# Optimization experiments

Measured on AMD Instinct MI355X. Metric: run time of the kernel, lower is better.

Reference implementation:

```python
import jax, jax.numpy as jnp
import numpy as np

B, S, D, H = 4, 2048, 512, 8
HD = D // H  # head_dim = 64


def setup_inputs() -> dict:
    key = jax.random.key(0)
    ks = jax.random.split(key, 16)
    sd = 1.0 / np.sqrt(D)
    def lin(ka, kb):
        W = jax.random.uniform(ka, (D, D), jnp.float32, -sd, sd)
        b = jax.random.uniform(kb, (D,), jnp.float32, -sd, sd)
        return W, b
    Wq, bq = lin(ks[0], ks[1])
    Wk, bk = lin(ks[2], ks[3])
    Wv, bv = lin(ks[4], ks[5])
    Wo, bo = lin(ks[6], ks[7])
    Ws, bs = lin(ks[8], ks[9])
    Wsh, bsh = lin(ks[10], ks[11])
    mod1_feat = jax.random.normal(ks[12], (B, S, D), jnp.float32)
    mod2_feat = jax.random.normal(ks[13], (B, S, D), jnp.float32)
    return {"mod1_feat": mod1_feat, "mod2_feat": mod2_feat,
            "Wq": Wq, "bq": bq, "Wk": Wk, "bk": bk, "Wv": Wv, "bv": bv,
            "Wo": Wo, "bo": bo, "Ws": Ws, "bs": bs, "Wsh": Wsh, "bsh": bsh}


def _heads(x):
    # [B, S, D] -> [B, H, S, HD]
    b, s, _ = x.shape
    return x.reshape(b, s, H, HD).transpose(0, 2, 1, 3)


def reference(mod1_feat, mod2_feat, Wq, bq, Wk, bk, Wv, bv, Wo, bo, Ws, bs, Wsh, bsh):
    Q = _heads(mod1_feat @ Wq + bq)
    K = _heads(mod2_feat @ Wk + bk)
    V = _heads(mod2_feat @ Wv + bv)
    scale = _heads(mod2_feat @ Ws + bs)
    shift = _heads(mod2_feat @ Wsh + bsh)
    K = K * scale + shift
    V = V * scale + shift
    scores = jnp.einsum('bhqd,bhkd->bhqk', Q, K) / jnp.sqrt(jnp.float32(HD))
    attn = jax.nn.softmax(scores, axis=-1)
    out = jnp.einsum('bhqk,bhkd->bhqd', attn, V)  # [B, H, S, HD]
    out = out.transpose(0, 2, 1, 3).reshape(mod1_feat.shape[0], -1, H * HD)
    return out @ Wo + bo
```

## Files before the change

### kernel.cpp

```cpp
#include <hip/hip_runtime.h>
#include <hip/hip_bf16.h>
#include <cstdint>
#include <cstddef>

typedef __bf16 bf16_t;
typedef __bf16 bf16x8 __attribute__((ext_vector_type(8)));
typedef __bf16 bf16x4 __attribute__((ext_vector_type(4)));
typedef float f32x4 __attribute__((ext_vector_type(4)));

#define DEVINL static __device__ __forceinline__

constexpr int B_ = 4, S_ = 2048, D_ = 512, H_ = 8, HD_ = 64;
constexpr int M_ = B_ * S_;
constexpr int NIN = 14;

DEVINL bf16x8 load8g(const bf16_t* p) { return *reinterpret_cast<const bf16x8*>(p); }

DEVINL int swcol(int col, int row) {
  return (col & ~63) | ((((col >> 3) ^ row) & 7) << 3) | (col & 7);
}

DEVINL int pK(int row) { return (row & 3) | (((row >> 3) & 1) << 2); }
DEVINL int swcolK(int col, int row) {
  return (col & ~63) | ((((col >> 3) ^ pK(row)) & 7) << 3) | (col & 7);
}

DEVINL void gl2lds(const bf16_t* g, bf16_t* l) {
  __builtin_amdgcn_global_load_lds(
      (const __attribute__((address_space(1))) void*)g,
      (__attribute__((address_space(3))) void*)l, 16, 0, 0);
}

DEVINL void stage16(bf16_t* dst, const void* src, size_t off, bool f32) {
  if (f32) {
    const float* p = (const float*)src + off;
    bf16x8 v0, v1;
#pragma unroll
    for (int j = 0; j < 8; ++j) { v0[j] = (bf16_t)p[j]; v1[j] = (bf16_t)p[8 + j]; }
    *reinterpret_cast<bf16x8*>(dst)     = v0;
    *reinterpret_cast<bf16x8*>(dst + 8) = v1;
  } else {
    const bf16_t* p = (const bf16_t*)src + off;
    *reinterpret_cast<bf16x8*>(dst)     = load8g(p);
    *reinterpret_cast<bf16x8*>(dst + 8) = load8g(p + 8);
  }
}

DEVINL float readf(const void* p, size_t i, bool f32) {
  return f32 ? ((const float*)p)[i] : (float)((const bf16_t*)p)[i];
}

struct DetectArgs { const uint16_t* p[NIN]; int n[NIN]; int* flags; };

__global__ __launch_bounds__(64) void detect_kernel(DetectArgs a) {
  const int z = blockIdx.x;
  const uint16_t* p = a.p[z];
  const int n = a.n[z];
  const int t = threadIdx.x;
  int cnt = 0;
  for (int i = t; i < n; i += 64) {
    const int e = (p[i] >> 7) & 0xFF;
    cnt += (e >= 200);
  }
#pragma unroll
  for (int off = 32; off > 0; off >>= 1) cnt += __shfl_down(cnt, off, 64);
  if (t == 0) a.flags[z] = (cnt > 16) ? 1 : 0;
}

struct CvtArgs { const void* src[2]; bf16_t* dst[2]; int idx[2]; const int* flags; };

__global__ __launch_bounds__(256) void cvt_kernel(CvtArgs a) {
  const int z = blockIdx.y;
  const bool f32 = a.flags[a.idx[z]] != 0;
  const size_t i = ((size_t)blockIdx.x * 256 + threadIdx.x) * 8;
  const int row = (int)(i >> 9);
  const int col = (int)(i & 511);
  bf16_t* dst = a.dst[z] + (size_t)row * 512 + swcol(col, row);
  if (f32) {
    const float* p = (const float*)a.src[z] + i;
    bf16x8 v;
#pragma unroll
    for (int j = 0; j < 8; ++j) v[j] = (bf16_t)p[j];
    *reinterpret_cast<bf16x8*>(dst) = v;
  } else {
    *reinterpret_cast<bf16x8*>(dst) = load8g((const bf16_t*)a.src[z] + i);
  }
}

struct TransArgs { const void* src[6]; int srcIdx[6]; bf16_t* dst[6]; const int* flags; };

__global__ __launch_bounds__(256) void transpose_kernel(TransArgs a) {
  __shared__ bf16_t tile[64][80];
  const int w = blockIdx.z;
  const void* src = a.src[w];
  const bool f32 = a.flags[a.srcIdx[w]] != 0;
  bf16_t* dst = a.dst[w];
  const int k0 = blockIdx.x * 64, n0 = blockIdx.y * 64;
  const int t = threadIdx.x;
  const int r = t >> 2, c0 = (t & 3) * 16;
  stage16(&tile[r][c0], src, (size_t)(k0 + r) * 512 + n0 + c0, f32);
  __syncthreads();
  const int orow = n0 + r;
  bf16_t* o = dst + (size_t)orow * 512;
#pragma unroll
  for (int half = 0; half < 2; ++half) {
    bf16x8 ov;
#pragma unroll
    for (int j = 0; j < 8; ++j) ov[j] = tile[c0 + half * 8 + j][r];
    *reinterpret_cast<bf16x8*>(o + swcol(k0 + c0 + half * 8, orow)) = ov;
  }
}

struct GemmBatch {
  const bf16_t* A[3];
  const bf16_t* Bt[3];
  const void* bias[3]; int bIdx[3];
  void* C[3];          int cIdx[3];
  const int* flags;
};

__global__ __launch_bounds__(512) void gemm_bt_kernel(GemmBatch args) {
  constexpr int K = 512, N = 512;
  __shared__ bf16_t As[3][128][64];
  __shared__ bf16_t Bs[3][64][64];
  const int z = blockIdx.z;
  const bf16_t* Ag  = args.A[z];
  const bf16_t* Btg = args.Bt[z];
  const int m0 = blockIdx.x * 128, n0 = blockIdx.y * 64;
  const int t = threadIdx.x, lane = t & 63, wave = t >> 6;
  const int l16 = lane & 15, quad = lane >> 4;
  const int wm = wave * 16;
  const int lr = lane >> 3, lc = (lane & 7) * 8;

  auto stage = [&](int slot, int k0) {
#pragma unroll
    for (int s = 0; s < 2; ++s) {
      const int r = wm + s * 8;
      gl2lds(Ag + (size_t)(m0 + r + lr) * K + k0 + lc, &As[slot][r][0]);
    }
    gl2lds(Btg + (size_t)(n0 + wave * 8 + lr) * K + k0 + lc, &Bs[slot][wave * 8][0]);
  };

  f32x4 acc[4] = {};

  stage(0, 0);
  stage(1, 64);

  constexpr int NT = K / 64;
  int cur = 0;
  for (int kt = 0; kt < NT - 1; ++kt) {
    asm volatile("s_waitcnt vmcnt(3)\n\ts_barrier" ::: "memory");
    __builtin_amdgcn_sched_barrier(0);
    if (kt + 2 < NT) {
      const int slot2 = cur == 0 ? 2 : cur - 1;
      stage(slot2, (kt + 2) * 64);
    }
#pragma unroll
    for (int ks = 0; ks < 2; ++ks) {
      const int sw = swcol(ks * 32 + quad * 8, l16);
      bf16x8 af = *reinterpret_cast<const bf16x8*>(&As[cur][wm + l16][sw]);
      bf16x8 bfr[4];
#pragma unroll
      for (int j = 0; j < 4; ++j)
        bfr[j] = *reinterpret_cast<const bf16x8*>(&Bs[cur][j * 16 + l16][sw]);
#pragma unroll
      for (int j = 0; j < 4; ++j)
        acc[j] = __builtin_amdgcn_mfma_f32_16x16x32_bf16(af, bfr[j], acc[j], 0, 0, 0);
    }
    cur = (cur == 2) ? 0 : cur + 1;
  }
  asm volatile("s_waitcnt vmcnt(0)\n\ts_barrier" ::: "memory");
  __builtin_amdgcn_sched_barrier(0);
#pragma unroll
  for (int ks = 0; ks < 2; ++ks) {
    const int sw = swcol(ks * 32 + quad * 8, l16);
    bf16x8 af = *reinterpret_cast<const bf16x8*>(&As[cur][wm + l16][sw]);
    bf16x8 bfr[4];
#pragma unroll
    for (int j = 0; j < 4; ++j)
      bfr[j] = *reinterpret_cast<const bf16x8*>(&Bs[cur][j * 16 + l16][sw]);
#pragma unroll
    for (int j = 0; j < 4; ++j)
      acc[j] = __builtin_amdgcn_mfma_f32_16x16x32_bf16(af, bfr[j], acc[j], 0, 0, 0);
  }

  const void* biag = args.bias[z];
  void* Cg         = args.C[z];
  const bool bf32 = args.bIdx[z] >= 0 && args.flags[args.bIdx[z]];
  const bool cf32 = args.cIdx[z] >= 0 && args.flags[args.cIdx[z]];
#pragma unroll
  for (int j = 0; j < 4; ++j) {
    const int col = n0 + j * 16 + l16;
    const float bv = readf(biag, col, bf32);
    const int rowb = m0 + wm + quad * 4;
#pragma unroll
    for (int r = 0; r < 4; ++r) {
      const size_t idx = (size_t)(rowb + r) * N + col;
      const float v = acc[j][r] + bv;
      if (cf32) ((float*)Cg)[idx] = v;
      else      ((bf16_t*)Cg)[idx] = (bf16_t)v;
    }
  }
}

struct GemmModArgs {
  const bf16_t* A;
  const bf16_t* Bt[2];
  const void* bias[2]; int bIdx[2];
  const bf16_t* Sc;
  const bf16_t* Sh;
  bf16_t* Kmod;
  bf16_t* VtT;
  const int* flags;
};

__global__ __launch_bounds__(512) void gemm_mod_kernel(GemmModArgs args) {
  constexpr int K = 512;
  __shared__ bf16_t As[3][128][64];
  __shared__ bf16_t Bs[3][64][64];
  const int z = blockIdx.z;
  const bf16_t* Ag  = args.A;
  const bf16_t* Btg = args.Bt[z];
  const int m0 = blockIdx.x * 128, n0 = blockIdx.y * 64;
  const int t = threadIdx.x, lane = t & 63, wave = t >> 6;
  const int l16 = lane & 15, quad = lane >> 4;
  const int wm = wave * 16;
  const int lr = lane >> 3, lc = (lane & 7) * 8;

  auto stage = [&](int slot, int k0) {
#pragma unroll
    for (int s = 0; s < 2; ++s) {
      const int r = wm + s * 8;
      gl2lds(Ag + (size_t)(m0 + r + lr) * K + k0 + lc, &As[slot][r][0]);
    }
    gl2lds(Btg + (size_t)(n0 + wave * 8 + lr) * K + k0 + lc, &Bs[slot][wave * 8][0]);
  };

  f32x4 acc[4] = {};

  stage(0, 0);
  stage(1, 64);

  constexpr int NT = K / 64;
  int cur = 0;
  for (int kt = 0; kt < NT - 1; ++kt) {
    asm volatile("s_waitcnt vmcnt(3)\n\ts_barrier" ::: "memory");
    __builtin_amdgcn_sched_barrier(0);
    if (kt + 2 < NT) {
      const int slot2 = cur == 0 ? 2 : cur - 1;
      stage(slot2, (kt + 2) * 64);
    }
#pragma unroll
    for (int ks = 0; ks < 2; ++ks) {
      const int sw = swcol(ks * 32 + quad * 8, l16);
      bf16x8 af = *reinterpret_cast<const bf16x8*>(&As[cur][wm + l16][sw]);
      bf16x8 bfr[4];
#pragma unroll
      for (int j = 0; j < 4; ++j)
        bfr[j] = *reinterpret_cast<const bf16x8*>(&Bs[cur][j * 16 + l16][sw]);
#pragma unroll
      for (int j = 0; j < 4; ++j)
        acc[j] = __builtin_amdgcn_mfma_f32_16x16x32_bf16(af, bfr[j], acc[j], 0, 0, 0);
    }
    cur = (cur == 2) ? 0 : cur + 1;
  }
  asm volatile("s_waitcnt vmcnt(0)\n\ts_barrier" ::: "memory");
  __builtin_amdgcn_sched_barrier(0);
#pragma unroll
  for (int ks = 0; ks < 2; ++ks) {
    const int sw = swcol(ks * 32 + quad * 8, l16);
    bf16x8 af = *reinterpret_cast<const bf16x8*>(&As[cur][wm + l16][sw]);
    bf16x8 bfr[4];
#pragma unroll
    for (int j = 0; j < 4; ++j)
      bfr[j] = *reinterpret_cast<const bf16x8*>(&Bs[cur][j * 16 + l16][sw]);
#pragma unroll
    for (int j = 0; j < 4; ++j)
      acc[j] = __builtin_amdgcn_mfma_f32_16x16x32_bf16(af, bfr[j], acc[j], 0, 0, 0);
  }

  const void* biag = args.bias[z];
  const bool bf32 = args.bIdx[z] >= 0 && args.flags[args.bIdx[z]];
#pragma unroll
  for (int j = 0; j < 4; ++j) {
    const int col = n0 + j * 16 + l16;
    const float bv = readf(biag, col, bf32);
    const int rowb = m0 + wm + quad * 4;
    if (z == 0) {
#pragma unroll
      for (int r = 0; r < 4; ++r) {
        const int row = rowb + r;
        const size_t idx = (size_t)row * 512 + col;
        const float sc = (float)args.Sc[idx], sh = (float)args.Sh[idx];
        args.Kmod[(size_t)row * 512 + swcolK(col, row)] = (bf16_t)fmaf(acc[j][r] + bv, sc, sh);
      }
    } else {
      bf16x4 pack;
#pragma unroll
      for (int r = 0; r < 4; ++r) {
        const size_t idx = (size_t)(rowb + r) * 512 + col;
        const float sc = (float)args.Sc[idx], sh = (float)args.Sh[idx];
        pack[r] = (bf16_t)fmaf(acc[j][r] + bv, sc, sh);
      }
      const int bb = rowb >> 11;
      const int ss = rowb & 2047;
      const int hh = col >> 6, dd = col & 63;
      *reinterpret_cast<bf16x4*>(
          args.VtT + (((size_t)(bb * H_ + hh)) * HD_ + dd) * S_ + swcol(ss, dd)) = pack;
    }
  }
}

__global__ __launch_bounds__(512) void attn_kernel(const bf16_t* Q, const bf16_t* Kb,
                                                   const bf16_t* Vt, bf16_t* O) {
  __shared__ bf16_t Ks[3][64][64];
  __shared__ bf16_t Vs[3][64][64];
  const int i = blockIdx.x;
  const int xcd = i & 7, g = i >> 3;
  const int slice = xcd * 4 + (g & 3);
  const int qt = g >> 2;
  const int b = slice >> 3, h = slice & 7;
  const int t = threadIdx.x, wave = t >> 6, lane = t & 63;
  const int l16 = lane & 15, quad = lane >> 4;
  const int q0 = qt * 128 + wave * 16;
  const int lr = lane >> 3, lc = (lane & 7) * 8;

  bf16x8 ones;
#pragma unroll
  for (int j = 0; j < 8; ++j) ones[j] = (bf16_t)1.0f;

  bf16x8 qf[2];
  {
    const size_t qrow = ((size_t)b * S_ + q0 + l16) * D_ + h * HD_;
    qf[0] = load8g(Q + qrow + quad * 8);
    qf[1] = load8g(Q + qrow + 32 + quad * 8);
  }

  f32x4 oacc[4] = {};
  f32x4 lacc = {};

  const size_t kbase = (size_t)b * S_ * D_ + h * HD_;
  const size_t vbase = ((size_t)(b * H_ + h)) * HD_ * S_;

  const int rbase = ((l16 >> 2) << 3) | (l16 & 3);
  int koff[2][4];
#pragma unroll
  for (int j = 0; j < 4; ++j) {
    const int rho = rbase + (j >> 1) * 32 + (j & 1) * 4;
#pragma unroll
    for (int dc = 0; dc < 2; ++dc)
      koff[dc][j] = rho * 64 + swcolK(dc * 32 + quad * 8, rho);
  }
  const int voff[2] = { swcol(quad * 8, l16), swcol(32 + quad * 8, l16) };

  auto stage = [&](int slot, int k0) {
    const int r = wave * 8;
    gl2lds(Kb + kbase + (size_t)(k0 + r + lr) * D_ + lc, &Ks[slot][r][0]);
    gl2lds(Vt + vbase + (size_t)(r + lr) * S_ + k0 + lc, &Vs[slot][r][0]);
  };

  constexpr float CE = 0.18033688011112042f;

  auto compute = [&](int cur) {
    f32x4 sacc[4] = {};
    const bf16_t* ksbase = &Ks[cur][0][0];
#pragma unroll
    for (int dc = 0; dc < 2; ++dc) {
      bf16x8 kf[4];
#pragma unroll
      for (int j = 0; j < 4; ++j)
        kf[j] = *reinterpret_cast<const bf16x8*>(ksbase + koff[dc][j]);
#pragma unroll
      for (int j = 0; j < 4; ++j)
        sacc[j] = __builtin_amdgcn_mfma_f32_16x16x32_bf16(kf[j], qf[dc], sacc[j], 0, 0, 0);
    }
#pragma unroll
    for (int kc = 0; kc < 2; ++kc) {
      bf16x8 vf[4];
#pragma unroll
      for (int dj = 0; dj < 4; ++dj)
        vf[dj] = *reinterpret_cast<const bf16x8*>(&Vs[cur][dj * 16 + l16][voff[kc]]);
      bf16x8 bp;
#pragma unroll
      for (int r = 0; r < 4; ++r) {
        bp[r]     = (bf16_t)__builtin_amdgcn_exp2f(fminf(sacc[kc * 2][r]     * CE, 57.5f));
        bp[4 + r] = (bf16_t)__builtin_amdgcn_exp2f(fminf(sacc[kc * 2 + 1][r] * CE, 57.5f));
      }
#pragma unroll
      for (int dj = 0; dj < 4; ++dj)
        oacc[dj] = __builtin_amdgcn_mfma_f32_16x16x32_bf16(vf[dj], bp, oacc[dj], 0, 0, 0);
      lacc = __builtin_amdgcn_mfma_f32_16x16x32_bf16(ones, bp, lacc, 0, 0, 0);
    }
  };

  asm volatile("s_waitcnt vmcnt(0)" ::: "memory");
  stage(0, 0);
  stage(1, 64);

  constexpr int NT = S_ / 64;
  int cur = 0;
  for (int kt = 0; kt < NT - 1; ++kt) {
    asm volatile("s_waitcnt vmcnt(2)\n\ts_barrier" ::: "memory");
    __builtin_amdgcn_sched_barrier(0);
    if (kt + 2 < NT) {
      const int slot2 = cur == 0 ? 2 : cur - 1;
      stage(slot2, (kt + 2) * 64);
    }
    compute(cur);
    cur = (cur == 2) ? 0 : cur + 1;
  }
  asm volatile("s_waitcnt vmcnt(0)\n\ts_barrier" ::: "memory");
  __builtin_amdgcn_sched_barrier(0);
  compute(cur);

  {
    const float linv = 1.0f / fmaxf(lacc[0], 1e-30f);
    const int q = q0 + l16;
    const size_t orow = ((size_t)b * S_ + q) * D_ + h * HD_;
#pragma unroll
    for (int dj = 0; dj < 4; ++dj) {
      bf16x4 pack;
#pragma unroll
      for (int r = 0; r < 4; ++r) pack[r] = (bf16_t)(oacc[dj][r] * linv);
      *reinterpret_cast<bf16x4*>(&O[orow + swcol(dj * 16 + quad * 4, q)]) = pack;
    }
  }
}

extern "C" void kernel_launch(void* const* d_in, const int* in_sizes, int n_in,
                              void* d_out, int out_size, void* d_ws, size_t ws_size,
                              hipStream_t stream) {
  (void)n_in; (void)out_size; (void)ws_size;

  char* ws = (char*)d_ws;
  auto alloc = [&](size_t bytes) -> char* {
    char* p = ws; ws += (bytes + 255) & ~(size_t)255; return p;
  };
  int* flags = (int*)alloc(64 * sizeof(int));
  const size_t wbytes = (size_t)512 * 512 * sizeof(bf16_t);
  const size_t fbytes = (size_t)M_ * D_ * sizeof(bf16_t);
  bf16_t* wt    = (bf16_t*)alloc(6 * wbytes);
  bf16_t* m1b   = (bf16_t*)alloc(fbytes);
  bf16_t* m2b   = (bf16_t*)alloc(fbytes);
  bf16_t* q_buf = (bf16_t*)alloc(fbytes);
  bf16_t* stmp  = (bf16_t*)alloc(fbytes);
  bf16_t* shtmp = (bf16_t*)alloc(fbytes);
  bf16_t* kmod  = (bf16_t*)alloc(fbytes);
  bf16_t* vtb    = m1b;
  bf16_t* attn_b = stmp;

  bf16_t* wtq  = wt + 0 * 512 * 512;
  bf16_t* wtk  = wt + 1 * 512 * 512;
  bf16_t* wtv  = wt + 2 * 512 * 512;
  bf16_t* wts  = wt + 3 * 512 * 512;
  bf16_t* wtsh = wt + 4 * 512 * 512;
  bf16_t* wto  = wt + 5 * 512 * 512;

  DetectArgs da;
  for (int i = 0; i < NIN; ++i) {
    da.p[i] = (const uint16_t*)d_in[i];
    da.n[i] = in_sizes[i] < 2048 ? in_sizes[i] : 2048;
  }
  da.flags = flags;
  hipLaunchKernelGGL(detect_kernel, dim3(NIN), dim3(64), 0, stream, da);

  CvtArgs ca;
  ca.src[0] = d_in[0]; ca.dst[0] = m1b; ca.idx[0] = 0;
  ca.src[1] = d_in[1]; ca.dst[1] = m2b; ca.idx[1] = 1;
  ca.flags = flags;
  hipLaunchKernelGGL(cvt_kernel, dim3(M_ * D_ / 2048, 2), dim3(256), 0, stream, ca);

  TransArgs ta;
  const int widx[6] = {2, 4, 6, 10, 12, 8};
  bf16_t* wdst[6] = {wtq, wtk, wtv, wts, wtsh, wto};
  for (int i = 0; i < 6; ++i) { ta.src[i] = d_in[widx[i]]; ta.srcIdx[i] = widx[i]; ta.dst[i] = wdst[i]; }
  ta.flags = flags;
  hipLaunchKernelGGL(transpose_kernel, dim3(8, 8, 6), dim3(256), 0, stream, ta);

  GemmBatch g1;
  g1.A[0] = m1b; g1.A[1] = m2b; g1.A[2] = m2b;
  g1.Bt[0] = wtq; g1.Bt[1] = wts; g1.Bt[2] = wtsh;
  g1.bias[0] = d_in[3];  g1.bIdx[0] = 3;
  g1.bias[1] = d_in[11]; g1.bIdx[1] = 11;
  g1.bias[2] = d_in[13]; g1.bIdx[2] = 13;
  g1.C[0] = q_buf; g1.cIdx[0] = -1;
  g1.C[1] = stmp;  g1.cIdx[1] = -1;
  g1.C[2] = shtmp; g1.cIdx[2] = -1;
  g1.flags = flags;
  hipLaunchKernelGGL(gemm_bt_kernel, dim3(M_ / 128, 8, 3), dim3(512), 0, stream, g1);

  GemmModArgs gm;
  gm.A = m2b;
  gm.Bt[0] = wtk; gm.Bt[1] = wtv;
  gm.bias[0] = d_in[5]; gm.bIdx[0] = 5;
  gm.bias[1] = d_in[7]; gm.bIdx[1] = 7;
  gm.Sc = stmp; gm.Sh = shtmp;
  gm.Kmod = kmod; gm.VtT = vtb;
  gm.flags = flags;
  hipLaunchKernelGGL(gemm_mod_kernel, dim3(M_ / 128, 8, 2), dim3(512), 0, stream, gm);

  hipLaunchKernelGGL(attn_kernel, dim3(512), dim3(512), 0, stream,
                     q_buf, kmod, vtb, attn_b);

  GemmBatch g2;
  for (int i = 0; i < 3; ++i) {
    g2.A[i] = attn_b;
    g2.Bt[i] = wto;
    g2.bias[i] = d_in[9]; g2.bIdx[i] = 9;
    g2.C[i] = d_out; g2.cIdx[i] = 0;
  }
  g2.flags = flags;
  hipLaunchKernelGGL(gemm_bt_kernel, dim3(M_ / 128, 8, 1), dim3(512), 0, stream, g2);
}
```

Measured before the change: 215.3 us.

## Fuse K, V, scale and shift projections into one GEMM with in-register modulation

```diff
diff --git a/kernel.cpp b/kernel.cpp
--- a/kernel.cpp
+++ b/kernel.cpp
@@ -203,40 +203,42 @@
   }
 }
 
-struct GemmModArgs {
+struct KsvArgs {
   const bf16_t* A;
-  const bf16_t* Bt[2];
-  const void* bias[2]; int bIdx[2];
-  const bf16_t* Sc;
-  const bf16_t* Sh;
+  const bf16_t* Bt[4];
+  const void* bias[4]; int bIdx[4];
   bf16_t* Kmod;
   bf16_t* VtT;
   const int* flags;
 };
 
-__global__ __launch_bounds__(512) void gemm_mod_kernel(GemmModArgs args) {
+__global__ __launch_bounds__(512) void ksv_kernel(KsvArgs args) {
   constexpr int K = 512;
   __shared__ bf16_t As[3][128][64];
-  __shared__ bf16_t Bs[3][64][64];
-  const int z = blockIdx.z;
-  const bf16_t* Ag  = args.A;
-  const bf16_t* Btg = args.Bt[z];
+  __shared__ bf16_t Bs[3][4][64][64];
   const int m0 = blockIdx.x * 128, n0 = blockIdx.y * 64;
   const int t = threadIdx.x, lane = t & 63, wave = t >> 6;
   const int l16 = lane & 15, quad = lane >> 4;
-  const int wm = wave * 16;
+  const int wm = (wave >> 2) * 64;
+  const int wn = (wave & 3) * 16;
   const int lr = lane >> 3, lc = (lane & 7) * 8;
 
   auto stage = [&](int slot, int k0) {
 #pragma unroll
     for (int s = 0; s < 2; ++s) {
-      const int r = wm + s * 8;
-      gl2lds(Ag + (size_t)(m0 + r + lr) * K + k0 + lc, &As[slot][r][0]);
-    }
-    gl2lds(Btg + (size_t)(n0 + wave * 8 + lr) * K + k0 + lc, &Bs[slot][wave * 8][0]);
+      const int r = wave * 16 + s * 8;
+      gl2lds(args.A + (size_t)(m0 + r + lr) * K + k0 + lc, &As[slot][r][0]);
+    }
+    const int mat = wave >> 1;
+    const int rb = (wave & 1) * 32;
+#pragma unroll
+    for (int s = 0; s < 4; ++s) {
+      const int r = rb + s * 8;
+      gl2lds(args.Bt[mat] + (size_t)(n0 + r + lr) * K + k0 + lc, &Bs[slot][mat][r][0]);
+    }
   };
 
-  f32x4 acc[4] = {};
+  f32x4 acc[4][4] = {};
 
   stage(0, 0);
   stage(1, 64);
@@ -244,7 +246,7 @@
   constexpr int NT = K / 64;
   int cur = 0;
   for (int kt = 0; kt < NT - 1; ++kt) {
-    asm volatile("s_waitcnt vmcnt(3)\n\ts_barrier" ::: "memory");
+    asm volatile("s_waitcnt vmcnt(6)\n\ts_barrier" ::: "memory");
     __builtin_amdgcn_sched_barrier(0);
     if (kt + 2 < NT) {
       const int slot2 = cur == 0 ? 2 : cur - 1;
@@ -253,14 +255,18 @@
 #pragma unroll
     for (int ks = 0; ks < 2; ++ks) {
       const int sw = swcol(ks * 32 + quad * 8, l16);
-      bf16x8 af = *reinterpret_cast<const bf16x8*>(&As[cur][wm + l16][sw]);
-      bf16x8 bfr[4];
-#pragma unroll
-      for (int j = 0; j < 4; ++j)
-        bfr[j] = *reinterpret_cast<const bf16x8*>(&Bs[cur][j * 16 + l16][sw]);
-#pragma unroll
-      for (int j = 0; j < 4; ++j)
-        acc[j] = __builtin_amdgcn_mfma_f32_16x16x32_bf16(af, bfr[j], acc[j], 0, 0, 0);
+      bf16x8 af[4], bfr[4];
+#pragma unroll
+      for (int mi = 0; mi < 4; ++mi)
+        af[mi] = *reinterpret_cast<const bf16x8*>(&As[cur][wm + mi * 16 + l16][sw]);
+#pragma unroll
+      for (int mat = 0; mat < 4; ++mat)
+        bfr[mat] = *reinterpret_cast<const bf16x8*>(&Bs[cur][mat][wn + l16][sw]);
+#pragma unroll
+      for (int mat = 0; mat < 4; ++mat)
+#pragma unroll
+        for (int mi = 0; mi < 4; ++mi)
+          acc[mat][mi] = __builtin_amdgcn_mfma_f32_16x16x32_bf16(af[mi], bfr[mat], acc[mat][mi], 0, 0, 0);
     }
     cur = (cur == 2) ? 0 : cur + 1;
   }
@@ -269,45 +275,44 @@
 #pragma unroll
   for (int ks = 0; ks < 2; ++ks) {
     const int sw = swcol(ks * 32 + quad * 8, l16);
-    bf16x8 af = *reinterpret_cast<const bf16x8*>(&As[cur][wm + l16][sw]);
-    bf16x8 bfr[4];
-#pragma unroll
-    for (int j = 0; j < 4; ++j)
-      bfr[j] = *reinterpret_cast<const bf16x8*>(&Bs[cur][j * 16 + l16][sw]);
-#pragma unroll
-    for (int j = 0; j < 4; ++j)
-      acc[j] = __builtin_amdgcn_mfma_f32_16x16x32_bf16(af, bfr[j], acc[j], 0, 0, 0);
-  }
-
-  const void* biag = args.bias[z];
-  const bool bf32 = args.bIdx[z] >= 0 && args.flags[args.bIdx[z]];
-#pragma unroll
-  for (int j = 0; j < 4; ++j) {
-    const int col = n0 + j * 16 + l16;
-    const float bv = readf(biag, col, bf32);
-    const int rowb = m0 + wm + quad * 4;
-    if (z == 0) {
-#pragma unroll
-      for (int r = 0; r < 4; ++r) {
-        const int row = rowb + r;
-        const size_t idx = (size_t)row * 512 + col;
-        const float sc = (float)args.Sc[idx], sh = (float)args.Sh[idx];
-        args.Kmod[(size_t)row * 512 + swcolK(col, row)] = (bf16_t)fmaf(acc[j][r] + bv, sc, sh);
-      }
-    } else {
-      bf16x4 pack;
-#pragma unroll
-      for (int r = 0; r < 4; ++r) {
-        const size_t idx = (size_t)(rowb + r) * 512 + col;
-        const float sc = (float)args.Sc[idx], sh = (float)args.Sh[idx];
-        pack[r] = (bf16_t)fmaf(acc[j][r] + bv, sc, sh);
-      }
-      const int bb = rowb >> 11;
-      const int ss = rowb & 2047;
-      const int hh = col >> 6, dd = col & 63;
-      *reinterpret_cast<bf16x4*>(
-          args.VtT + (((size_t)(bb * H_ + hh)) * HD_ + dd) * S_ + swcol(ss, dd)) = pack;
-    }
+    bf16x8 af[4], bfr[4];
+#pragma unroll
+    for (int mi = 0; mi < 4; ++mi)
+      af[mi] = *reinterpret_cast<const bf16x8*>(&As[cur][wm + mi * 16 + l16][sw]);
+#pragma unroll
+    for (int mat = 0; mat < 4; ++mat)
+      bfr[mat] = *reinterpret_cast<const bf16x8*>(&Bs[cur][mat][wn + l16][sw]);
+#pragma unroll
+    for (int mat = 0; mat < 4; ++mat)
+#pragma unroll
+      for (int mi = 0; mi < 4; ++mi)
+        acc[mat][mi] = __builtin_amdgcn_mfma_f32_16x16x32_bf16(af[mi], bfr[mat], acc[mat][mi], 0, 0, 0);
+  }
+
+  const int col = n0 + wn + l16;
+  const float bk  = readf(args.bias[0], col, args.bIdx[0] >= 0 && args.flags[args.bIdx[0]]);
+  const float bv  = readf(args.bias[1], col, args.bIdx[1] >= 0 && args.flags[args.bIdx[1]]);
+  const float bs  = readf(args.bias[2], col, args.bIdx[2] >= 0 && args.flags[args.bIdx[2]]);
+  const float bsh = readf(args.bias[3], col, args.bIdx[3] >= 0 && args.flags[args.bIdx[3]]);
+  const int hh = col >> 6, dd = col & 63;
+#pragma unroll
+  for (int mi = 0; mi < 4; ++mi) {
+    const int rowb = m0 + wm + mi * 16 + quad * 4;
+    bf16x4 vpack;
+#pragma unroll
+    for (int r = 0; r < 4; ++r) {
+      const int row = rowb + r;
+      const float s  = acc[2][mi][r] + bs;
+      const float sh = acc[3][mi][r] + bsh;
+      const float kk = fmaf(acc[0][mi][r] + bk, s, sh);
+      const float vv = fmaf(acc[1][mi][r] + bv, s, sh);
+      args.Kmod[(size_t)row * 512 + swcolK(col, row)] = (bf16_t)kk;
+      vpack[r] = (bf16_t)vv;
+    }
+    const int bb = rowb >> 11;
+    const int ss = rowb & 2047;
+    *reinterpret_cast<bf16x4*>(
+        args.VtT + (((size_t)(bb * H_ + hh)) * HD_ + dd) * S_ + swcol(ss, dd)) = vpack;
   }
 }
 
@@ -443,11 +448,10 @@
   bf16_t* m1b   = (bf16_t*)alloc(fbytes);
   bf16_t* m2b   = (bf16_t*)alloc(fbytes);
   bf16_t* q_buf = (bf16_t*)alloc(fbytes);
-  bf16_t* stmp  = (bf16_t*)alloc(fbytes);
-  bf16_t* shtmp = (bf16_t*)alloc(fbytes);
+  bf16_t* atmp  = (bf16_t*)alloc(fbytes);
   bf16_t* kmod  = (bf16_t*)alloc(fbytes);
   bf16_t* vtb    = m1b;
-  bf16_t* attn_b = stmp;
+  bf16_t* attn_b = atmp;
 
   bf16_t* wtq  = wt + 0 * 512 * 512;
   bf16_t* wtk  = wt + 1 * 512 * 512;
@@ -478,26 +482,27 @@
   hipLaunchKernelGGL(transpose_kernel, dim3(8, 8, 6), dim3(256), 0, stream, ta);
 
   GemmBatch g1;
-  g1.A[0] = m1b; g1.A[1] = m2b; g1.A[2] = m2b;
-  g1.Bt[0] = wtq; g1.Bt[1] = wts; g1.Bt[2] = wtsh;
+  g1.A[0] = m1b;  g1.A[1] = m1b;  g1.A[2] = m1b;
+  g1.Bt[0] = wtq; g1.Bt[1] = wtq; g1.Bt[2] = wtq;
   g1.bias[0] = d_in[3];  g1.bIdx[0] = 3;
-  g1.bias[1] = d_in[11]; g1.bIdx[1] = 11;
-  g1.bias[2] = d_in[13]; g1.bIdx[2] = 13;
+  g1.bias[1] = d_in[3];  g1.bIdx[1] = 3;
+  g1.bias[2] = d_in[3];  g1.bIdx[2] = 3;
   g1.C[0] = q_buf; g1.cIdx[0] = -1;
-  g1.C[1] = stmp;  g1.cIdx[1] = -1;
-  g1.C[2] = shtmp; g1.cIdx[2] = -1;
+  g1.C[1] = q_buf; g1.cIdx[1] = -1;
+  g1.C[2] = q_buf; g1.cIdx[2] = -1;
   g1.flags = flags;
-  hipLaunchKernelGGL(gemm_bt_kernel, dim3(M_ / 128, 8, 3), dim3(512), 0, stream, g1);
-
-  GemmModArgs gm;
-  gm.A = m2b;
-  gm.Bt[0] = wtk; gm.Bt[1] = wtv;
-  gm.bias[0] = d_in[5]; gm.bIdx[0] = 5;
-  gm.bias[1] = d_in[7]; gm.bIdx[1] = 7;
-  gm.Sc = stmp; gm.Sh = shtmp;
-  gm.Kmod = kmod; gm.VtT = vtb;
-  gm.flags = flags;
-  hipLaunchKernelGGL(gemm_mod_kernel, dim3(M_ / 128, 8, 2), dim3(512), 0, stream, gm);
+  hipLaunchKernelGGL(gemm_bt_kernel, dim3(M_ / 128, 8, 1), dim3(512), 0, stream, g1);
+
+  KsvArgs kv;
+  kv.A = m2b;
+  kv.Bt[0] = wtk; kv.Bt[1] = wtv; kv.Bt[2] = wts; kv.Bt[3] = wtsh;
+  kv.bias[0] = d_in[5];  kv.bIdx[0] = 5;
+  kv.bias[1] = d_in[7];  kv.bIdx[1] = 7;
+  kv.bias[2] = d_in[11]; kv.bIdx[2] = 11;
+  kv.bias[3] = d_in[13]; kv.bIdx[3] = 13;
+  kv.Kmod = kmod; kv.VtT = vtb;
+  kv.flags = flags;
+  hipLaunchKernelGGL(ksv_kernel, dim3(M_ / 128, 8), dim3(512), 0, stream, kv);
 
   hipLaunchKernelGGL(attn_kernel, dim3(512), dim3(512), 0, stream,
                      q_buf, kmod, vtb, attn_b);
```

Result: faster. 201.8 us (-6.3%).
